# Kernel tuning notes

Hardware: AMD Instinct MI355X
Metric: run time of the kernel (lower is better)

## Reference

```python
import jax, jax.numpy as jnp
import numpy as np

N_DRUG = 846
E = 256          # embedding_num
NS = 128         # neighbor_sample_size
N_ENT = 100000
N_REL = 200
BN_EPS = 1e-5


def setup_inputs() -> dict:
    key = jax.random.key(0)
    ks = jax.random.split(key, 12)
    return {
        "gnn1_embedding": jax.random.normal(ks[0], (N_DRUG, E), jnp.float32),
        "idx": 0,
        "drug_name": jnp.arange(N_DRUG, dtype=jnp.int64),
        "adj_tail": jax.random.randint(ks[1], (N_DRUG, NS), 0, N_ENT, dtype=jnp.int64),
        "adj_relation": jax.random.randint(ks[2], (N_DRUG, NS), 0, N_REL, dtype=jnp.int64),
        "drug_table": jax.random.normal(ks[3], (N_DRUG, E), jnp.float32),
        "rela_table": jax.random.normal(ks[4], (N_REL, E), jnp.float32),
        "ent_table": jax.random.normal(ks[5], (N_ENT, E), jnp.float32),
        "W1": jax.random.normal(ks[6], (N_DRUG, E, E), jnp.float32) * 0.05,
        "b1": jax.random.normal(ks[7], (NS, E), jnp.float32) * 0.05,
        "W2": jax.random.normal(ks[8], (N_DRUG, E, E), jnp.float32) * 0.05,
        "b2": jax.random.normal(ks[9], (NS, E), jnp.float32) * 0.05,
        "lin_w": jax.random.normal(ks[10], (2 * E, E), jnp.float32) * (1.0 / np.sqrt(2 * E)),
        "lin_b": jnp.zeros((E,), jnp.float32),
        "bn_gamma": jnp.ones((E,), jnp.float32),
        "bn_beta": jnp.zeros((E,), jnp.float32),
    }


def reference(gnn1_embedding, idx, drug_name, adj_tail, adj_relation,
              drug_table, rela_table, ent_table,
              W1, b1, W2, b2, lin_w, lin_b, bn_gamma, bn_beta):
    d = drug_table[drug_name]            # [846, E]
    r = rela_table[adj_relation]         # [846, NS, E]
    t = ent_table[adj_tail]              # [846, NS, E]

    dr = d[:, None, :] * r               # [846, NS, E]
    h = jnp.einsum('bne,bef->bnf', dr, W1) + b1   # per-drug batched matmul
    h = jax.nn.relu(h)
    h = jnp.einsum('bne,bef->bnf', h, W2) + b2
    score = jnp.sum(h, axis=-1)          # [846, NS]
    attn = jax.nn.softmax(score, axis=1) # softmax over neighbors

    weighted_ent = jnp.einsum('bn,bne->be', attn, t)   # [846, E]
    drug_e = jnp.concatenate([weighted_ent, d], axis=1)  # [846, 2E]

    x = drug_e @ lin_w + lin_b
    x = jax.nn.relu(x)
    # BatchNorm1d in training mode: biased batch stats over the drug axis
    mean = jnp.mean(x, axis=0)
    var = jnp.mean((x - mean) ** 2, axis=0)
    drug_f = (x - mean) * jax.lax.rsqrt(var + BN_EPS) * bn_gamma + bn_beta
    return (drug_f, gnn1_embedding, idx)
```

## Files before the change

kernel.cpp:

```cpp
#include <hip/hip_runtime.h>
#include <hip/hip_bf16.h>

#define NDRUG 846
#define EDIM 256
#define NS 128

typedef short s8v __attribute__((ext_vector_type(8)));
typedef __bf16 b8v __attribute__((ext_vector_type(8)));
typedef float f32x4 __attribute__((ext_vector_type(4)));

static __device__ __forceinline__ short bfs(float f) {
  __bf16 h = (__bf16)f;
  return __builtin_bit_cast(short, h);
}

template <typename V>
static __device__ __forceinline__ auto mfma_impl(V a, V b, f32x4 c, int)
    -> decltype(__builtin_amdgcn_mfma_f32_16x16x32_bf16(a, b, c, 0, 0, 0)) {
  return __builtin_amdgcn_mfma_f32_16x16x32_bf16(a, b, c, 0, 0, 0);
}
template <typename V>
static __device__ __forceinline__ f32x4 mfma_impl(V a, V b, f32x4 c, long) {
  b8v ab = __builtin_bit_cast(b8v, a);
  b8v bb = __builtin_bit_cast(b8v, b);
  return __builtin_amdgcn_mfma_f32_16x16x32_bf16(ab, bb, c, 0, 0, 0);
}
static __device__ __forceinline__ f32x4 mfma16(s8v a, s8v b, f32x4 c) {
  return mfma_impl(a, b, c, 0);
}

__global__ __launch_bounds__(512, 4) void gnn_main(
    const int* __restrict__ drug_name,
    const int* __restrict__ adj_tail,
    const int* __restrict__ adj_relation,
    const float* __restrict__ drug_table,
    const float* __restrict__ rela_table,
    const float* __restrict__ ent_table,
    const float* __restrict__ W1,
    const float* __restrict__ b1,
    const float* __restrict__ W2,
    const float* __restrict__ b2,
    const float* __restrict__ lin_w,
    const float* __restrict__ lin_b,
    float* __restrict__ xT) {
  __shared__ __align__(16) unsigned short s_ab[NS * EDIM];
  __shared__ float s_d[EDIM];
  __shared__ int s_tail[NS];
  __shared__ float s_w2sum[EDIM];
  __shared__ float s_b2sum[NS];
  __shared__ float s_scorep[8][NS];
  __shared__ float s_attn[NS];

  const int b = blockIdx.x;
  const int tid = threadIdx.x;
  const int w = tid >> 6;
  const int l = tid & 63;
  const int g = l >> 4;
  const int lr = l & 15;

  if (tid < EDIM) {
    const int dn = drug_name[b];
    s_d[tid] = drug_table[(long)dn * EDIM + tid];
  } else if (tid < EDIM + NS) {
    s_tail[tid - EDIM] = adj_tail[b * NS + (tid - EDIM)];
  }

  {
    const int rg = tid >> 4;
    const int lc = (tid & 15) * 16;
    const float* W2p = W2 + (long)b * EDIM * EDIM;
#pragma unroll
    for (int s = 0; s < 8; ++s) {
      const int e = 32 * s + rg;
      const float* p = W2p + e * EDIM + lc;
      float4 a0 = *(const float4*)p, a1 = *(const float4*)(p + 4);
      float4 a2 = *(const float4*)(p + 8), a3 = *(const float4*)(p + 12);
      float v = a0.x + a0.y + a0.z + a0.w + a1.x + a1.y + a1.z + a1.w +
                a2.x + a2.y + a2.z + a2.w + a3.x + a3.y + a3.z + a3.w;
#pragma unroll
      for (int off = 1; off < 16; off <<= 1) v += __shfl_xor(v, off);
      if ((tid & 15) == 0) s_w2sum[e] = v;
    }
#pragma unroll
    for (int s = 0; s < 4; ++s) {
      const int n = 32 * s + rg;
      const float* p = b2 + n * EDIM + lc;
      float4 a0 = *(const float4*)p, a1 = *(const float4*)(p + 4);
      float4 a2 = *(const float4*)(p + 8), a3 = *(const float4*)(p + 12);
      float v = a0.x + a0.y + a0.z + a0.w + a1.x + a1.y + a1.z + a1.w +
                a2.x + a2.y + a2.z + a2.w + a3.x + a3.y + a3.z + a3.w;
#pragma unroll
      for (int off = 1; off < 16; off <<= 1) v += __shfl_xor(v, off);
      if ((tid & 15) == 0) s_b2sum[n] = v;
    }
  }
  __syncthreads();

  {
    const int n = tid >> 2;
    const int e0 = (tid & 3) * 64;
    const int rel = adj_relation[b * NS + n];
    const float* rrow = rela_table + (long)rel * EDIM;
    const int swz = (n & 7) << 4;
#pragma unroll
    for (int c = 0; c < 8; ++c) {
      const int e = e0 + c * 8;
      float4 p0 = *(const float4*)(rrow + e);
      float4 p1 = *(const float4*)(rrow + e + 4);
      s8v v;
      v[0] = bfs(p0.x * s_d[e + 0]);
      v[1] = bfs(p0.y * s_d[e + 1]);
      v[2] = bfs(p0.z * s_d[e + 2]);
      v[3] = bfs(p0.w * s_d[e + 3]);
      v[4] = bfs(p1.x * s_d[e + 4]);
      v[5] = bfs(p1.y * s_d[e + 5]);
      v[6] = bfs(p1.z * s_d[e + 6]);
      v[7] = bfs(p1.w * s_d[e + 7]);
      *(s8v*)((char*)s_ab + ((n * 512 + e * 2) ^ swz)) = v;
    }
  }
  __syncthreads();

  f32x4 acc[8][2];
#pragma unroll
  for (int mt = 0; mt < 8; ++mt) {
    acc[mt][0] = (f32x4){0.f, 0.f, 0.f, 0.f};
    acc[mt][1] = (f32x4){0.f, 0.f, 0.f, 0.f};
  }
  {
    const float* Wp = W1 + (long)b * EDIM * EDIM;
    const int col0 = 32 * w + lr;
    const int swz = (lr & 7) << 4;
    float fb[2][16];
    s8v bf0[2], bf1[2];

#define LOADW(buf, kt)                                      \
  do {                                                      \
    const float* pk = Wp + ((kt)*32 + 8 * g) * EDIM + col0; \
    _Pragma("unroll") for (int j = 0; j < 8; ++j) {         \
      (buf)[j] = pk[j * EDIM];                              \
      (buf)[8 + j] = pk[j * EDIM + 16];                     \
    }                                                       \
  } while (0)
#define CVTW(d0, d1, src)                           \
  do {                                              \
    _Pragma("unroll") for (int j = 0; j < 8; ++j) { \
      (d0)[j] = bfs((src)[j]);                      \
      (d1)[j] = bfs((src)[8 + j]);                  \
    }                                               \
  } while (0)

    LOADW(fb[0], 0);
    LOADW(fb[1], 1);
    CVTW(bf0[0], bf1[0], fb[0]);

#pragma unroll
    for (int kk = 0; kk < 8; ++kk) {
      const int c = kk & 1;
      if (kk + 2 < 8) LOADW(fb[c], kk + 2);
      const int kb = (32 * kk + 8 * g) * 2;
#pragma unroll
      for (int mt = 0; mt < 8; ++mt) {
        const int row = 16 * mt + lr;
        s8v af = *(const s8v*)((const char*)s_ab + ((row * 512 + kb) ^ swz));
        acc[mt][0] = mfma16(af, c ? bf0[1] : bf0[0], acc[mt][0]);
        acc[mt][1] = mfma16(af, c ? bf1[1] : bf1[0], acc[mt][1]);
      }
      if (kk + 1 < 8) {
        if (c)
          CVTW(bf0[0], bf1[0], fb[0]);
        else
          CVTW(bf0[1], bf1[1], fb[1]);
      }
    }
#undef LOADW
#undef CVTW
  }

#pragma unroll
  for (int mt = 0; mt < 8; ++mt) {
#pragma unroll
    for (int jj = 0; jj < 4; ++jj) {
      const int n = 16 * mt + 4 * g + jj;
      const int f0 = 32 * w + lr;
      const int f1 = f0 + 16;
      float v = fmaxf(acc[mt][0][jj] + b1[n * EDIM + f0], 0.f) * s_w2sum[f0] +
                fmaxf(acc[mt][1][jj] + b1[n * EDIM + f1], 0.f) * s_w2sum[f1];
#pragma unroll
      for (int off = 1; off < 16; off <<= 1) v += __shfl_xor(v, off);
      if (lr == 0) s_scorep[w][n] = v;
    }
  }
  __syncthreads();

  if (w == 0) {
    float v0 = s_b2sum[l], v1 = s_b2sum[l + 64];
#pragma unroll
    for (int ww = 0; ww < 8; ++ww) {
      v0 += s_scorep[ww][l];
      v1 += s_scorep[ww][l + 64];
    }
    float m = fmaxf(v0, v1);
#pragma unroll
    for (int off = 1; off < 64; off <<= 1) m = fmaxf(m, __shfl_xor(m, off));
    const float e0 = expf(v0 - m), e1 = expf(v1 - m);
    float s = e0 + e1;
#pragma unroll
    for (int off = 1; off < 64; off <<= 1) s += __shfl_xor(s, off);
    const float inv = 1.f / s;
    s_attn[l] = e0 * inv;
    s_attn[l + 64] = e1 * inv;
  }
  __syncthreads();

  float* s_scratch = (float*)s_ab;
  float* s_we = (float*)s_ab + 2048;
  float* s_lin = (float*)s_ab + 2304;

  {
    const int f4 = tid & 63;
    const int ng = tid >> 6;
    float4 a = {0.f, 0.f, 0.f, 0.f};
#pragma unroll 8
    for (int i = 0; i < 16; ++i) {
      const int n = 16 * ng + i;
      const float4 e4 = *(const float4*)(ent_table + (long)s_tail[n] * EDIM + 4 * f4);
      const float at = s_attn[n];
      a.x += at * e4.x;
      a.y += at * e4.y;
      a.z += at * e4.z;
      a.w += at * e4.w;
    }
    *(float4*)(s_scratch + ng * 256 + 4 * f4) = a;
  }
  __syncthreads();

  if (tid < EDIM) {
    float v = 0.f;
#pragma unroll
    for (int ng = 0; ng < 8; ++ng) v += s_scratch[ng * 256 + tid];
    s_we[tid] = v;
  }
  __syncthreads();

  {
    const int f = tid & 255;
    const int half = tid >> 8;
    const float* wp = lin_w + (long)half * EDIM * EDIM + f;
    const float* src = half ? s_d : s_we;
    float a0 = 0.f, a1 = 0.f, a2 = 0.f, a3 = 0.f;
#pragma unroll 8
    for (int e = 0; e < 64; ++e) {
      a0 += src[e] * wp[(long)e * EDIM];
      a1 += src[e + 64] * wp[(long)(e + 64) * EDIM];
      a2 += src[e + 128] * wp[(long)(e + 128) * EDIM];
      a3 += src[e + 192] * wp[(long)(e + 192) * EDIM];
    }
    s_lin[half * EDIM + f] = (a0 + a1) + (a2 + a3);
  }
  __syncthreads();

  if (tid < EDIM) {
    float x = s_lin[tid] + s_lin[EDIM + tid] + lin_b[tid];
    x = fmaxf(x, 0.f);
    xT[tid * NDRUG + b] = x;
  }
}

__global__ __launch_bounds__(256) void bn_kernel(const float* __restrict__ xT,
                                                 const float* __restrict__ gamma,
                                                 const float* __restrict__ beta,
                                                 float* __restrict__ out) {
  const int f = blockIdx.x;
  const int t = threadIdx.x;
  const float* col = xT + f * NDRUG;
  float s = 0.f, ss = 0.f;
  for (int i = t; i < NDRUG; i += 256) {
    const float v = col[i];
    s += v;
    ss += v * v;
  }
#pragma unroll
  for (int off = 1; off < 64; off <<= 1) {
    s += __shfl_xor(s, off);
    ss += __shfl_xor(ss, off);
  }
  __shared__ float as_[4], ass_[4];
  if ((t & 63) == 0) {
    as_[t >> 6] = s;
    ass_[t >> 6] = ss;
  }
  __syncthreads();
  s = as_[0] + as_[1] + as_[2] + as_[3];
  ss = ass_[0] + ass_[1] + ass_[2] + ass_[3];
  const float mean = s * (1.f / NDRUG);
  const float var = ss * (1.f / NDRUG) - mean * mean;
  const float sc = rsqrtf(var + 1e-5f) * gamma[f];
  const float sh = beta[f] - mean * sc;
  for (int i = t; i < NDRUG; i += 256) out[i * EDIM + f] = col[i] * sc + sh;
}

__global__ void tail_kernel(const float* __restrict__ gnn1, const int* __restrict__ idx,
                            float* __restrict__ out) {
  const int total4 = NDRUG * EDIM / 4;
  const float4* s4 = (const float4*)gnn1;
  float4* d4 = (float4*)(out + NDRUG * EDIM);
  for (int i = blockIdx.x * blockDim.x + threadIdx.x; i < total4;
       i += gridDim.x * blockDim.x)
    d4[i] = s4[i];
  if (blockIdx.x == 0 && threadIdx.x == 0) out[2 * NDRUG * EDIM] = (float)idx[0];
}

extern "C" void kernel_launch(void* const* d_in, const int* in_sizes, int n_in,
                              void* d_out, int out_size, void* d_ws, size_t ws_size,
                              hipStream_t stream) {
  const float* gnn1       = (const float*)d_in[0];
  const int*   idx        = (const int*)d_in[1];
  const int*   drug_name  = (const int*)d_in[2];
  const int*   adj_tail   = (const int*)d_in[3];
  const int*   adj_rel    = (const int*)d_in[4];
  const float* drug_table = (const float*)d_in[5];
  const float* rela_table = (const float*)d_in[6];
  const float* ent_table  = (const float*)d_in[7];
  const float* W1         = (const float*)d_in[8];
  const float* b1         = (const float*)d_in[9];
  const float* W2         = (const float*)d_in[10];
  const float* b2         = (const float*)d_in[11];
  const float* lin_w      = (const float*)d_in[12];
  const float* lin_b      = (const float*)d_in[13];
  const float* bn_g       = (const float*)d_in[14];
  const float* bn_b       = (const float*)d_in[15];

  float* out = (float*)d_out;
  float* xT  = (float*)d_ws;

  gnn_main<<<NDRUG, 512, 0, stream>>>(drug_name, adj_tail, adj_rel, drug_table,
                                      rela_table, ent_table, W1, b1, W2, b2,
                                      lin_w, lin_b, xT);
  bn_kernel<<<EDIM, 256, 0, stream>>>(xT, bn_g, bn_b, out);
  tail_kernel<<<240, 256, 0, stream>>>(gnn1, idx, out);
}
```

Baseline: 166.3 us.

## Split final linear into batched MFMA GEMM and overlap W2 row-sums with W1 GEMM

The per-drug dense matvec against lin_w moves out of gnn_main into a separate bf16 MFMA GEMM kernel that processes 64 drugs per block. This stops every block from re-reading the full lin_w matrix. The W2 row-sum loads are interleaved into the W1 MFMA loop so the streaming overlaps with compute, and the b2 row sum is precomputed once by a tiny kernel. BatchNorm is split into parallel stats, finalize and apply kernels, and the entity gather uses two accumulators. The price is more kernel launches, bf16 rounding in the final linear, and reuse of the output buffer as scratch space.

Result: slower. 246.2 us (+48.0%).

```diff
diff --git a/kernel.cpp b/kernel.cpp
--- a/kernel.cpp
+++ b/kernel.cpp
@@ -4,6 +4,10 @@
 #define NDRUG 846
 #define EDIM 256
 #define NS 128
+#define XOFF (NDRUG * EDIM)
+#define B2SOFF (2 * NDRUG * EDIM - NS)
+#define NLINBLK 14
+#define NSTATBLK 54
 
 typedef short s8v __attribute__((ext_vector_type(8)));
 typedef __bf16 b8v __attribute__((ext_vector_type(8)));
@@ -27,6 +31,17 @@
 }
 static __device__ __forceinline__ f32x4 mfma16(s8v a, s8v b, f32x4 c) {
   return mfma_impl(a, b, c, 0);
+}
+
+__global__ __launch_bounds__(64) void b2prep(const float* __restrict__ b2,
+                                             float* __restrict__ b2s) {
+  const int n = blockIdx.x;
+  const int t = threadIdx.x;
+  const float4 v4 = *(const float4*)(b2 + n * EDIM + 4 * t);
+  float v = v4.x + v4.y + v4.z + v4.w;
+#pragma unroll
+  for (int off = 1; off < 64; off <<= 1) v += __shfl_xor(v, off);
+  if (t == 0) b2s[n] = v;
 }
 
 __global__ __launch_bounds__(512, 4) void gnn_main(
@@ -39,15 +54,12 @@
     const float* __restrict__ W1,
     const float* __restrict__ b1,
     const float* __restrict__ W2,
-    const float* __restrict__ b2,
-    const float* __restrict__ lin_w,
-    const float* __restrict__ lin_b,
-    float* __restrict__ xT) {
+    const float* __restrict__ b2s,
+    float* __restrict__ ws_we) {
   __shared__ __align__(16) unsigned short s_ab[NS * EDIM];
   __shared__ float s_d[EDIM];
   __shared__ int s_tail[NS];
   __shared__ float s_w2sum[EDIM];
-  __shared__ float s_b2sum[NS];
   __shared__ float s_scorep[8][NS];
   __shared__ float s_attn[NS];
 
@@ -57,42 +69,14 @@
   const int l = tid & 63;
   const int g = l >> 4;
   const int lr = l & 15;
+  const int rg = tid >> 4;
+  const int lc = tid & 15;
 
   if (tid < EDIM) {
     const int dn = drug_name[b];
     s_d[tid] = drug_table[(long)dn * EDIM + tid];
   } else if (tid < EDIM + NS) {
     s_tail[tid - EDIM] = adj_tail[b * NS + (tid - EDIM)];
-  }
-
-  {
-    const int rg = tid >> 4;
-    const int lc = (tid & 15) * 16;
-    const float* W2p = W2 + (long)b * EDIM * EDIM;
-#pragma unroll
-    for (int s = 0; s < 8; ++s) {
-      const int e = 32 * s + rg;
-      const float* p = W2p + e * EDIM + lc;
-      float4 a0 = *(const float4*)p, a1 = *(const float4*)(p + 4);
-      float4 a2 = *(const float4*)(p + 8), a3 = *(const float4*)(p + 12);
-      float v = a0.x + a0.y + a0.z + a0.w + a1.x + a1.y + a1.z + a1.w +
-                a2.x + a2.y + a2.z + a2.w + a3.x + a3.y + a3.z + a3.w;
-#pragma unroll
-      for (int off = 1; off < 16; off <<= 1) v += __shfl_xor(v, off);
-      if ((tid & 15) == 0) s_w2sum[e] = v;
-    }
-#pragma unroll
-    for (int s = 0; s < 4; ++s) {
-      const int n = 32 * s + rg;
-      const float* p = b2 + n * EDIM + lc;
-      float4 a0 = *(const float4*)p, a1 = *(const float4*)(p + 4);
-      float4 a2 = *(const float4*)(p + 8), a3 = *(const float4*)(p + 12);
-      float v = a0.x + a0.y + a0.z + a0.w + a1.x + a1.y + a1.z + a1.w +
-                a2.x + a2.y + a2.z + a2.w + a3.x + a3.y + a3.z + a3.w;
-#pragma unroll
-      for (int off = 1; off < 16; off <<= 1) v += __shfl_xor(v, off);
-      if ((tid & 15) == 0) s_b2sum[n] = v;
-    }
   }
   __syncthreads();
 
@@ -129,6 +113,7 @@
   }
   {
     const float* Wp = W1 + (long)b * EDIM * EDIM;
+    const float* W2p = W2 + (long)b * EDIM * EDIM;
     const int col0 = 32 * w + lr;
     const int swz = (lr & 7) << 4;
     float fb[2][16];
@@ -157,25 +142,38 @@
 #pragma unroll
     for (int kk = 0; kk < 8; ++kk) {
       const int c = kk & 1;
+      const float* q = W2p + (32 * kk + rg) * EDIM + lc * 16;
+      const float4 q0 = *(const float4*)q;
+      const float4 q1 = *(const float4*)(q + 4);
+      const float4 q2 = *(const float4*)(q + 8);
+      const float4 q3 = *(const float4*)(q + 12);
       if (kk + 2 < 8) LOADW(fb[c], kk + 2);
+      __builtin_amdgcn_sched_barrier(0);
       const int kb = (32 * kk + 8 * g) * 2;
 #pragma unroll
       for (int mt = 0; mt < 8; ++mt) {
         const int row = 16 * mt + lr;
         s8v af = *(const s8v*)((const char*)s_ab + ((row * 512 + kb) ^ swz));
-        acc[mt][0] = mfma16(af, c ? bf0[1] : bf0[0], acc[mt][0]);
-        acc[mt][1] = mfma16(af, c ? bf1[1] : bf1[0], acc[mt][1]);
+        acc[mt][0] = mfma16(af, bf0[c], acc[mt][0]);
+        acc[mt][1] = mfma16(af, bf1[c], acc[mt][1]);
       }
+      __builtin_amdgcn_sched_barrier(0);
       if (kk + 1 < 8) {
         if (c)
           CVTW(bf0[0], bf1[0], fb[0]);
         else
           CVTW(bf0[1], bf1[1], fb[1]);
       }
+      float v = q0.x + q0.y + q0.z + q0.w + q1.x + q1.y + q1.z + q1.w +
+                q2.x + q2.y + q2.z + q2.w + q3.x + q3.y + q3.z + q3.w;
+#pragma unroll
+      for (int off = 1; off < 16; off <<= 1) v += __shfl_xor(v, off);
+      if (lc == 0) s_w2sum[32 * kk + rg] = v;
     }
 #undef LOADW
 #undef CVTW
   }
+  __syncthreads();
 
 #pragma unroll
   for (int mt = 0; mt < 8; ++mt) {
@@ -194,7 +192,7 @@
   __syncthreads();
 
   if (w == 0) {
-    float v0 = s_b2sum[l], v1 = s_b2sum[l + 64];
+    float v0 = b2s[l], v1 = b2s[l + 64];
 #pragma unroll
     for (int ww = 0; ww < 8; ++ww) {
       v0 += s_scorep[ww][l];
@@ -214,24 +212,22 @@
   __syncthreads();
 
   float* s_scratch = (float*)s_ab;
-  float* s_we = (float*)s_ab + 2048;
-  float* s_lin = (float*)s_ab + 2304;
-
   {
     const int f4 = tid & 63;
     const int ng = tid >> 6;
-    float4 a = {0.f, 0.f, 0.f, 0.f};
-#pragma unroll 8
-    for (int i = 0; i < 16; ++i) {
-      const int n = 16 * ng + i;
-      const float4 e4 = *(const float4*)(ent_table + (long)s_tail[n] * EDIM + 4 * f4);
-      const float at = s_attn[n];
-      a.x += at * e4.x;
-      a.y += at * e4.y;
-      a.z += at * e4.z;
-      a.w += at * e4.w;
-    }
-    *(float4*)(s_scratch + ng * 256 + 4 * f4) = a;
+    float4 a0 = {0.f, 0.f, 0.f, 0.f}, a1 = {0.f, 0.f, 0.f, 0.f};
+#pragma unroll
+    for (int i = 0; i < 8; ++i) {
+      const int n0 = 16 * ng + i;
+      const int n1 = n0 + 8;
+      const float4 e0 = *(const float4*)(ent_table + (long)s_tail[n0] * EDIM + 4 * f4);
+      const float4 e1 = *(const float4*)(ent_table + (long)s_tail[n1] * EDIM + 4 * f4);
+      const float t0 = s_attn[n0], t1 = s_attn[n1];
+      a0.x += t0 * e0.x; a0.y += t0 * e0.y; a0.z += t0 * e0.z; a0.w += t0 * e0.w;
+      a1.x += t1 * e1.x; a1.y += t1 * e1.y; a1.z += t1 * e1.z; a1.w += t1 * e1.w;
+    }
+    a0.x += a1.x; a0.y += a1.y; a0.z += a1.z; a0.w += a1.w;
+    *(float4*)(s_scratch + ng * 256 + 4 * f4) = a0;
   }
   __syncthreads();
 
@@ -239,72 +235,171 @@
     float v = 0.f;
 #pragma unroll
     for (int ng = 0; ng < 8; ++ng) v += s_scratch[ng * 256 + tid];
-    s_we[tid] = v;
-  }
-  __syncthreads();
+    ws_we[(long)b * EDIM + tid] = v;
+  }
+}
+
+__global__ __launch_bounds__(512, 4) void lin_gemm(
+    const float* __restrict__ ws_we,
+    const int* __restrict__ drug_name,
+    const float* __restrict__ drug_table,
+    const float* __restrict__ lin_w,
+    const float* __restrict__ lin_b,
+    float* __restrict__ x_out) {
+  __shared__ __align__(16) unsigned short s_a[64 * 512];
+  const int blk = blockIdx.x;
+  const int m0 = 64 * blk;
+  const int tid = threadIdx.x;
+  const int w = tid >> 6;
+  const int l = tid & 63;
+  const int g = l >> 4;
+  const int lr = l & 15;
 
   {
-    const int f = tid & 255;
-    const int half = tid >> 8;
-    const float* wp = lin_w + (long)half * EDIM * EDIM + f;
-    const float* src = half ? s_d : s_we;
-    float a0 = 0.f, a1 = 0.f, a2 = 0.f, a3 = 0.f;
-#pragma unroll 8
-    for (int e = 0; e < 64; ++e) {
-      a0 += src[e] * wp[(long)e * EDIM];
-      a1 += src[e + 64] * wp[(long)(e + 64) * EDIM];
-      a2 += src[e + 128] * wp[(long)(e + 128) * EDIM];
-      a3 += src[e + 192] * wp[(long)(e + 192) * EDIM];
-    }
-    s_lin[half * EDIM + f] = (a0 + a1) + (a2 + a3);
-  }
-  __syncthreads();
-
-  if (tid < EDIM) {
-    float x = s_lin[tid] + s_lin[EDIM + tid] + lin_b[tid];
-    x = fmaxf(x, 0.f);
-    xT[tid * NDRUG + b] = x;
-  }
-}
-
-__global__ __launch_bounds__(256) void bn_kernel(const float* __restrict__ xT,
-                                                 const float* __restrict__ gamma,
-                                                 const float* __restrict__ beta,
-                                                 float* __restrict__ out) {
-  const int f = blockIdx.x;
-  const int t = threadIdx.x;
-  const float* col = xT + f * NDRUG;
+    const int r = tid >> 3;
+    const int qq = tid & 7;
+    const int m = m0 + r;
+    const bool valid = m < NDRUG;
+    const int c0 = 64 * qq;
+    const float* src;
+    if (qq < 4) {
+      src = ws_we + (long)m * EDIM + c0;
+    } else {
+      const int dn = valid ? drug_name[m] : 0;
+      src = drug_table + (long)dn * EDIM + (c0 - EDIM);
+    }
+    const int swz = (r & 7) << 4;
+#pragma unroll
+    for (int u = 0; u < 8; ++u) {
+      float4 p0 = valid ? *(const float4*)(src + 8 * u)
+                        : (float4){0.f, 0.f, 0.f, 0.f};
+      float4 p1 = valid ? *(const float4*)(src + 8 * u + 4)
+                        : (float4){0.f, 0.f, 0.f, 0.f};
+      s8v v;
+      v[0] = bfs(p0.x); v[1] = bfs(p0.y); v[2] = bfs(p0.z); v[3] = bfs(p0.w);
+      v[4] = bfs(p1.x); v[5] = bfs(p1.y); v[6] = bfs(p1.z); v[7] = bfs(p1.w);
+      *(s8v*)((char*)s_a + ((r * 1024 + (c0 + 8 * u) * 2) ^ swz)) = v;
+    }
+  }
+  __syncthreads();
+
+  f32x4 acc[4][2];
+#pragma unroll
+  for (int mt = 0; mt < 4; ++mt) {
+    acc[mt][0] = (f32x4){0.f, 0.f, 0.f, 0.f};
+    acc[mt][1] = (f32x4){0.f, 0.f, 0.f, 0.f};
+  }
+  {
+    const int col0 = 32 * w + lr;
+    const int swz = (lr & 7) << 4;
+    float fb[2][16];
+    s8v bf0[2], bf1[2];
+#define LOADL(buf, kt)                                           \
+  do {                                                           \
+    const float* pk = lin_w + ((kt)*32 + 8 * g) * EDIM + col0;   \
+    _Pragma("unroll") for (int j = 0; j < 8; ++j) {              \
+      (buf)[j] = pk[j * EDIM];                                   \
+      (buf)[8 + j] = pk[j * EDIM + 16];                          \
+    }                                                            \
+  } while (0)
+#define CVTL(d0, d1, src)                           \
+  do {                                              \
+    _Pragma("unroll") for (int j = 0; j < 8; ++j) { \
+      (d0)[j] = bfs((src)[j]);                      \
+      (d1)[j] = bfs((src)[8 + j]);                  \
+    }                                               \
+  } while (0)
+    LOADL(fb[0], 0);
+    LOADL(fb[1], 1);
+    CVTL(bf0[0], bf1[0], fb[0]);
+#pragma unroll
+    for (int kk = 0; kk < 16; ++kk) {
+      const int c = kk & 1;
+      if (kk + 2 < 16) LOADL(fb[c], kk + 2);
+      __builtin_amdgcn_sched_barrier(0);
+      const int kb = (32 * kk + 8 * g) * 2;
+#pragma unroll
+      for (int mt = 0; mt < 4; ++mt) {
+        const int row = 16 * mt + lr;
+        s8v af = *(const s8v*)((const char*)s_a + ((row * 1024 + kb) ^ swz));
+        acc[mt][0] = mfma16(af, bf0[c], acc[mt][0]);
+        acc[mt][1] = mfma16(af, bf1[c], acc[mt][1]);
+      }
+      __builtin_amdgcn_sched_barrier(0);
+      if (kk + 1 < 16) {
+        if (c)
+          CVTL(bf0[0], bf1[0], fb[0]);
+        else
+          CVTL(bf0[1], bf1[1], fb[1]);
+      }
+    }
+#undef LOADL
+#undef CVTL
+  }
+
+#pragma unroll
+  for (int mt = 0; mt < 4; ++mt) {
+#pragma unroll
+    for (int nt = 0; nt < 2; ++nt) {
+      const int f = 32 * w + 16 * nt + lr;
+#pragma unroll
+      for (int jj = 0; jj < 4; ++jj) {
+        const int m = m0 + 16 * mt + 4 * g + jj;
+        if (m < NDRUG)
+          x_out[(long)m * EDIM + f] = fmaxf(acc[mt][nt][jj] + lin_b[f], 0.f);
+      }
+    }
+  }
+}
+
+__global__ __launch_bounds__(256) void bn_stats(const float* __restrict__ x,
+                                                float* __restrict__ part) {
+  const int mb = blockIdx.x * 16;
+  const int f = threadIdx.x;
   float s = 0.f, ss = 0.f;
-  for (int i = t; i < NDRUG; i += 256) {
-    const float v = col[i];
-    s += v;
-    ss += v * v;
-  }
-#pragma unroll
-  for (int off = 1; off < 64; off <<= 1) {
-    s += __shfl_xor(s, off);
-    ss += __shfl_xor(ss, off);
-  }
-  __shared__ float as_[4], ass_[4];
-  if ((t & 63) == 0) {
-    as_[t >> 6] = s;
-    ass_[t >> 6] = ss;
-  }
-  __syncthreads();
-  s = as_[0] + as_[1] + as_[2] + as_[3];
-  ss = ass_[0] + ass_[1] + ass_[2] + ass_[3];
+#pragma unroll
+  for (int i = 0; i < 16; ++i) {
+    const int m = mb + i;
+    if (m < NDRUG) {
+      const float v = x[(long)m * EDIM + f];
+      s += v;
+      ss += v * v;
+    }
+  }
+  part[blockIdx.x * 512 + f] = s;
+  part[blockIdx.x * 512 + 256 + f] = ss;
+}
+
+__global__ __launch_bounds__(256) void bn_finalize(const float* __restrict__ part,
+                                                   const float* __restrict__ gamma,
+                                                   const float* __restrict__ beta,
+                                                   float* __restrict__ scsh) {
+  const int f = threadIdx.x;
+  float s = 0.f, ss = 0.f;
+  for (int b = 0; b < NSTATBLK; ++b) {
+    s += part[b * 512 + f];
+    ss += part[b * 512 + 256 + f];
+  }
   const float mean = s * (1.f / NDRUG);
   const float var = ss * (1.f / NDRUG) - mean * mean;
   const float sc = rsqrtf(var + 1e-5f) * gamma[f];
-  const float sh = beta[f] - mean * sc;
-  for (int i = t; i < NDRUG; i += 256) out[i * EDIM + f] = col[i] * sc + sh;
+  scsh[f] = sc;
+  scsh[EDIM + f] = beta[f] - mean * sc;
+}
+
+__global__ __launch_bounds__(512) void bn_apply(const float* __restrict__ x,
+                                                const float* __restrict__ scsh,
+                                                float* __restrict__ out) {
+  const int i = blockIdx.x * 512 + threadIdx.x;
+  const int f = i & 255;
+  out[i] = x[i] * scsh[f] + scsh[EDIM + f];
 }
 
 __global__ void tail_kernel(const float* __restrict__ gnn1, const int* __restrict__ idx,
                             float* __restrict__ out) {
   const int total4 = NDRUG * EDIM / 4;
   const float4* s4 = (const float4*)gnn1;
-  float4* d4 = (float4*)(out + NDRUG * EDIM);
+  float4* d4 = (float4*)(out + XOFF);
   for (int i = blockIdx.x * blockDim.x + threadIdx.x; i < total4;
        i += gridDim.x * blockDim.x)
     d4[i] = s4[i];
@@ -332,11 +427,20 @@
   const float* bn_b       = (const float*)d_in[15];
 
   float* out = (float*)d_out;
-  float* xT  = (float*)d_ws;
-
+  float* x    = out + XOFF;
+  float* b2s  = out + B2SOFF;
+  float* part = out;
+  float* ws_we = (float*)d_ws;
+  float* scsh  = (float*)d_ws;
+
+  b2prep<<<NS, 64, 0, stream>>>(b2, b2s);
   gnn_main<<<NDRUG, 512, 0, stream>>>(drug_name, adj_tail, adj_rel, drug_table,
-                                      rela_table, ent_table, W1, b1, W2, b2,
-                                      lin_w, lin_b, xT);
-  bn_kernel<<<EDIM, 256, 0, stream>>>(xT, bn_g, bn_b, out);
+                                      rela_table, ent_table, W1, b1, W2, b2s,
+                                      ws_we);
+  lin_gemm<<<NLINBLK, 512, 0, stream>>>(ws_we, drug_name, drug_table, lin_w,
+                                        lin_b, x);
+  bn_stats<<<NSTATBLK, 256, 0, stream>>>(x, part);
+  bn_finalize<<<1, 256, 0, stream>>>(part, bn_g, bn_b, scsh);
+  bn_apply<<<(NDRUG * EDIM) / 512, 512, 0, stream>>>(x, scsh, out);
   tail_kernel<<<240, 256, 0, stream>>>(gnn1, idx, out);
 }
```
